# Kernel tuning notes

Hardware: AMD Instinct MI355X
Metric: run time of the kernel (lower is better)

## Reference

```python
import jax, jax.numpy as jnp
import numpy as np

TRAJ_STEPS = 1_000_000


def setup_inputs() -> dict:
    key = jax.random.key(0)
    k1, k2 = jax.random.split(key)
    start_pose = jax.random.normal(k1, (3,), dtype=jnp.float32)
    controls = jax.random.normal(k2, (TRAJ_STEPS, 2), dtype=jnp.float32)
    return {"start_pose": start_pose, "controls": controls}


def reference(start_pose, controls):
    # Unicycle rollout:
    #   traj[0]   = start_pose = (x0, y0, th0)
    #   traj[i+1] = traj[i] + (|u_i0|*cos(th_i), |u_i0|*sin(th_i), 10*u_i1)
    # theta evolves independently of x,y -> closed-form via cumsum.
    th0 = start_pose[2]
    dth = 10.0 * controls[:, 1]                      # (T,)
    th = th0 + jnp.cumsum(dth)                       # theta at steps 1..T
    th_prev = jnp.concatenate([th0[None], th[:-1]])  # theta at steps 0..T-1

    speed = jnp.abs(controls[:, 0])                  # (T,)
    dx = speed * jnp.cos(th_prev)
    dy = speed * jnp.sin(th_prev)
    x = start_pose[0] + jnp.cumsum(dx)               # x at steps 1..T
    y = start_pose[1] + jnp.cumsum(dy)

    traj_tail = jnp.stack([x, y, th], axis=1)        # (T, 3)
    traj = jnp.concatenate([start_pose[None, :], traj_tail], axis=0)  # (T+1, 3)
    return controls, traj
```

## Files before the change

kernel.cpp:

```cpp
#include <hip/hip_runtime.h>
#include <math.h>

#define T_STEPS 1000000
#define BLOCK 256
#define ITEMS 8
#define CHUNK (BLOCK * ITEMS)
#define NB ((T_STEPS + CHUNK - 1) / CHUNK)
#define NF4 (T_STEPS / 2)
#define PER 2


__device__ __forceinline__ double waveScanIncl(double v) {
#pragma unroll
    for (int off = 1; off < 64; off <<= 1) {
        double x = __shfl_up(v, off, 64);
        if ((threadIdx.x & 63) >= off) v += x;
    }
    return v;
}

__device__ __forceinline__ double blockScanEx(double v, double* sw, double* tot) {
    const int lane = threadIdx.x & 63, w = threadIdx.x >> 6;
    double inc = waveScanIncl(v);
    if (lane == 63) sw[w] = inc;
    __syncthreads();
    double w0 = sw[0], w1 = sw[1], w2 = sw[2], w3 = sw[3];
    __syncthreads();
    *tot = w0 + w1 + w2 + w3;
    double woff = (w > 0 ? w0 : 0.0) + (w > 1 ? w1 : 0.0) + (w > 2 ? w2 : 0.0);
    return woff + inc - v;
}

__device__ __forceinline__ double blockSum(double v, double* sw) {
#pragma unroll
    for (int off = 32; off > 0; off >>= 1) v += __shfl_xor(v, off, 64);
    const int lane = threadIdx.x & 63, w = threadIdx.x >> 6;
    if (lane == 0) sw[w] = v;
    __syncthreads();
    double r = sw[0] + sw[1] + sw[2] + sw[3];
    __syncthreads();
    return r;
}

__device__ __forceinline__ void ftrig(double th, double& cs, double& sn) {
    const double INV2PI = 0.15915494309189535;
    double rev = th * INV2PI;
    double fr = rev - rint(rev);
    float x = (float)fr * 6.283185307179586f;
    sn = (double)__sinf(x);
    cs = (double)__cosf(x);
}


__global__ void __launch_bounds__(BLOCK) k_agg(
    const float4* __restrict__ ctrl4, float4* __restrict__ out4,
    double* __restrict__ aggTh, double* __restrict__ aggA,
    double* __restrict__ aggB) {
    __shared__ double sw[4];
    const int b = blockIdx.x, t = threadIdx.x;
    const int f0 = b * (CHUNK / 2) + t * (ITEMS / 2);

    float4 c4[ITEMS / 2];
#pragma unroll
    for (int j = 0; j < ITEMS / 2; ++j) {
        int f = f0 + j;
        c4[j] = (f < NF4) ? ctrl4[f] : make_float4(0.f, 0.f, 0.f, 0.f);
    }
#pragma unroll
    for (int j = 0; j < ITEMS / 2; ++j) {
        int f = f0 + j;
        if (f < NF4) out4[f] = c4[j];
    }

    double dth[ITEMS];
    double lth = 0.0;
#pragma unroll
    for (int j = 0; j < ITEMS / 2; ++j) {
        dth[2 * j]     = 10.0 * (double)c4[j].y;
        dth[2 * j + 1] = 10.0 * (double)c4[j].w;
        lth += dth[2 * j] + dth[2 * j + 1];
    }
    double thTot;
    double thb = blockScanEx(lth, sw, &thTot);

    double la = 0.0, lb = 0.0;
    {
        double run = thb;
#pragma unroll
        for (int j = 0; j < ITEMS / 2; ++j) {
            double s0 = fabs((double)c4[j].x);
            double s1 = fabs((double)c4[j].z);
            double cs, sn;
            ftrig(run, cs, sn);
            la += s0 * cs; lb += s0 * sn;
            run += dth[2 * j];
            ftrig(run, cs, sn);
            la += s1 * cs; lb += s1 * sn;
            run += dth[2 * j + 1];
        }
    }
    double A = blockSum(la, sw);
    double B = blockSum(lb, sw);
    if (t == 0) {
        aggTh[b] = thTot;
        aggA[b]  = A;
        aggB[b]  = B;
    }
}


__global__ void __launch_bounds__(BLOCK) k_out(
    const float4* __restrict__ ctrl4, const float* __restrict__ sp,
    const double* __restrict__ aggTh, const double* __restrict__ aggA,
    const double* __restrict__ aggB, float* __restrict__ traj) {
    __shared__ double sw[4];
    const int b = blockIdx.x, t = threadIdx.x;

    const double x0 = (double)sp[0], y0 = (double)sp[1], th0 = (double)sp[2];

    double pTh[PER], pA[PER], pB[PER];
    double lsum = 0.0;
#pragma unroll
    for (int k = 0; k < PER; ++k) {
        int p = t * PER + k;
        if (p < NB) {
            pTh[k] = aggTh[p];
            pA[k]  = aggA[p];
            pB[k]  = aggB[p];
        } else {
            pTh[k] = pA[k] = pB[k] = 0.0;
        }
        lsum += pTh[k];
    }
    double dummyTot;
    double excl = blockScanEx(lsum, sw, &dummyTot);

    double cx = 0.0, cy = 0.0, mth = 0.0;
    {
        double run = th0 + excl;
#pragma unroll
        for (int k = 0; k < PER; ++k) {
            int p = t * PER + k;
            if (p < b) {
                double cs, sn;
                ftrig(run, cs, sn);
                cx += cs * pA[k] - sn * pB[k];
                cy += sn * pA[k] + cs * pB[k];
                mth += pTh[k];
            }
            run += pTh[k];
        }
    }
    const double psi = th0 + blockSum(mth, sw);
    const double Xin = x0 + blockSum(cx, sw);
    const double Yin = y0 + blockSum(cy, sw);
    double cps, sps;
    ftrig(psi, cps, sps);

    const int f0 = b * (CHUNK / 2) + t * (ITEMS / 2);
    float4 c4[ITEMS / 2];
#pragma unroll
    for (int j = 0; j < ITEMS / 2; ++j) {
        int f = f0 + j;
        c4[j] = (f < NF4) ? ctrl4[f] : make_float4(0.f, 0.f, 0.f, 0.f);
    }
    double dth[ITEMS];
    double lth = 0.0;
#pragma unroll
    for (int j = 0; j < ITEMS / 2; ++j) {
        dth[2 * j]     = 10.0 * (double)c4[j].y;
        dth[2 * j + 1] = 10.0 * (double)c4[j].w;
        lth += dth[2 * j] + dth[2 * j + 1];
    }
    double thTot;
    double thb = blockScanEx(lth, sw, &thTot);

    double av[ITEMS], bv[ITEMS];
    double la = 0.0, lb = 0.0;
    {
        double run = thb;
#pragma unroll
        for (int j = 0; j < ITEMS / 2; ++j) {
            double s0 = fabs((double)c4[j].x);
            double s1 = fabs((double)c4[j].z);
            double cs, sn;
            ftrig(run, cs, sn);
            av[2 * j] = s0 * cs; bv[2 * j] = s0 * sn;
            run += dth[2 * j];
            ftrig(run, cs, sn);
            av[2 * j + 1] = s1 * cs; bv[2 * j + 1] = s1 * sn;
            run += dth[2 * j + 1];
            la += av[2 * j] + av[2 * j + 1];
            lb += bv[2 * j] + bv[2 * j + 1];
        }
    }
    double aTot, bTot;
    double Ar = blockScanEx(la, sw, &aTot);
    double Br = blockScanEx(lb, sw, &bTot);

    {
        const long e0 = (long)b * CHUNK + (long)t * ITEMS;
        double run = thb;
#pragma unroll
        for (int k = 0; k < ITEMS; ++k) {
            Ar += av[k];
            Br += bv[k];
            run += dth[k];
            long i = e0 + k;
            if (i < T_STEPS) {
                float* row = traj + 3 * (i + 1);
                row[0] = (float)(Xin + cps * Ar - sps * Br);
                row[1] = (float)(Yin + sps * Ar + cps * Br);
                row[2] = (float)(psi + run);
            }
        }
    }
    if (b == 0 && t == 0) {
        traj[0] = sp[0];
        traj[1] = sp[1];
        traj[2] = sp[2];
    }
}


extern "C" void kernel_launch(void* const* d_in, const int* in_sizes, int n_in,
                              void* d_out, int out_size, void* d_ws, size_t ws_size,
                              hipStream_t stream) {
    const float*  start_pose = (const float*)d_in[0];
    const float4* ctrl4      = (const float4*)d_in[1];

    float*  out  = (float*)d_out;
    float4* out4 = (float4*)out;
    float*  traj = out + 2 * (long)T_STEPS;

    double* bsum  = (double*)d_ws;
    double* aggTh = bsum;
    double* aggA  = aggTh + NB;
    double* aggB  = aggA + NB;

    hipLaunchKernelGGL(k_agg, dim3(NB), dim3(BLOCK), 0, stream,
                       ctrl4, out4, aggTh, aggA, aggB);
    hipLaunchKernelGGL(k_out, dim3(NB), dim3(BLOCK), 0, stream,
                       ctrl4, start_pose, aggTh, aggA, aggB, traj);
}
```

Measured before the change: 23.46 us.

## Fuse aggregate and output kernels into one cooperative kernel with grid sync

Merges the two-pass scan (per-block aggregate kernel, then output kernel) into a single cooperative launch separated by a grid-wide sync. Each block keeps its controls, theta scan and per-element cos/sin products in registers across the sync, so the second pass no longer reloads controls or recomputes trig. This drops one kernel launch and the duplicated work. In exchange it relies on all 489 blocks being co-resident (launch_bounds with 2 blocks per CU) and pays the cost of a grid barrier.

```diff
diff --git a/kernel.cpp b/kernel.cpp
--- a/kernel.cpp
+++ b/kernel.cpp
@@ -1,5 +1,8 @@
 #include <hip/hip_runtime.h>
+#include <hip/hip_cooperative_groups.h>
 #include <math.h>
+
+namespace cg = cooperative_groups;
 
 #define T_STEPS 1000000
 #define BLOCK 256
@@ -52,8 +55,9 @@
 }
 
 
-__global__ void __launch_bounds__(BLOCK) k_agg(
-    const float4* __restrict__ ctrl4, float4* __restrict__ out4,
+__global__ void __launch_bounds__(BLOCK, 2) k_fused(
+    const float4* __restrict__ ctrl4, const float* __restrict__ sp,
+    float4* __restrict__ out4, float* __restrict__ traj,
     double* __restrict__ aggTh, double* __restrict__ aggA,
     double* __restrict__ aggB) {
     __shared__ double sw[4];
@@ -72,98 +76,6 @@
         if (f < NF4) out4[f] = c4[j];
     }
 
-    double dth[ITEMS];
-    double lth = 0.0;
-#pragma unroll
-    for (int j = 0; j < ITEMS / 2; ++j) {
-        dth[2 * j]     = 10.0 * (double)c4[j].y;
-        dth[2 * j + 1] = 10.0 * (double)c4[j].w;
-        lth += dth[2 * j] + dth[2 * j + 1];
-    }
-    double thTot;
-    double thb = blockScanEx(lth, sw, &thTot);
-
-    double la = 0.0, lb = 0.0;
-    {
-        double run = thb;
-#pragma unroll
-        for (int j = 0; j < ITEMS / 2; ++j) {
-            double s0 = fabs((double)c4[j].x);
-            double s1 = fabs((double)c4[j].z);
-            double cs, sn;
-            ftrig(run, cs, sn);
-            la += s0 * cs; lb += s0 * sn;
-            run += dth[2 * j];
-            ftrig(run, cs, sn);
-            la += s1 * cs; lb += s1 * sn;
-            run += dth[2 * j + 1];
-        }
-    }
-    double A = blockSum(la, sw);
-    double B = blockSum(lb, sw);
-    if (t == 0) {
-        aggTh[b] = thTot;
-        aggA[b]  = A;
-        aggB[b]  = B;
-    }
-}
-
-
-__global__ void __launch_bounds__(BLOCK) k_out(
-    const float4* __restrict__ ctrl4, const float* __restrict__ sp,
-    const double* __restrict__ aggTh, const double* __restrict__ aggA,
-    const double* __restrict__ aggB, float* __restrict__ traj) {
-    __shared__ double sw[4];
-    const int b = blockIdx.x, t = threadIdx.x;
-
-    const double x0 = (double)sp[0], y0 = (double)sp[1], th0 = (double)sp[2];
-
-    double pTh[PER], pA[PER], pB[PER];
-    double lsum = 0.0;
-#pragma unroll
-    for (int k = 0; k < PER; ++k) {
-        int p = t * PER + k;
-        if (p < NB) {
-            pTh[k] = aggTh[p];
-            pA[k]  = aggA[p];
-            pB[k]  = aggB[p];
-        } else {
-            pTh[k] = pA[k] = pB[k] = 0.0;
-        }
-        lsum += pTh[k];
-    }
-    double dummyTot;
-    double excl = blockScanEx(lsum, sw, &dummyTot);
-
-    double cx = 0.0, cy = 0.0, mth = 0.0;
-    {
-        double run = th0 + excl;
-#pragma unroll
-        for (int k = 0; k < PER; ++k) {
-            int p = t * PER + k;
-            if (p < b) {
-                double cs, sn;
-                ftrig(run, cs, sn);
-                cx += cs * pA[k] - sn * pB[k];
-                cy += sn * pA[k] + cs * pB[k];
-                mth += pTh[k];
-            }
-            run += pTh[k];
-        }
-    }
-    const double psi = th0 + blockSum(mth, sw);
-    const double Xin = x0 + blockSum(cx, sw);
-    const double Yin = y0 + blockSum(cy, sw);
-    double cps, sps;
-    ftrig(psi, cps, sps);
-
-    const int f0 = b * (CHUNK / 2) + t * (ITEMS / 2);
-    float4 c4[ITEMS / 2];
-#pragma unroll
-    for (int j = 0; j < ITEMS / 2; ++j) {
-        int f = f0 + j;
-        c4[j] = (f < NF4) ? ctrl4[f] : make_float4(0.f, 0.f, 0.f, 0.f);
-    }
     double dth[ITEMS];
     double lth = 0.0;
 #pragma unroll
@@ -194,6 +106,57 @@
             lb += bv[2 * j] + bv[2 * j + 1];
         }
     }
+    double A = blockSum(la, sw);
+    double B = blockSum(lb, sw);
+    if (t == 0) {
+        aggTh[b] = thTot;
+        aggA[b]  = A;
+        aggB[b]  = B;
+    }
+
+    cg::this_grid().sync();
+
+    const double x0 = (double)sp[0], y0 = (double)sp[1], th0 = (double)sp[2];
+
+    double pTh[PER], pA[PER], pB[PER];
+    double lsum = 0.0;
+#pragma unroll
+    for (int k = 0; k < PER; ++k) {
+        int p = t * PER + k;
+        if (p < NB) {
+            pTh[k] = aggTh[p];
+            pA[k]  = aggA[p];
+            pB[k]  = aggB[p];
+        } else {
+            pTh[k] = pA[k] = pB[k] = 0.0;
+        }
+        lsum += pTh[k];
+    }
+    double dummyTot;
+    double excl = blockScanEx(lsum, sw, &dummyTot);
+
+    double cx = 0.0, cy = 0.0, mth = 0.0;
+    {
+        double run2 = th0 + excl;
+#pragma unroll
+        for (int k = 0; k < PER; ++k) {
+            int p = t * PER + k;
+            if (p < b) {
+                double cs, sn;
+                ftrig(run2, cs, sn);
+                cx += cs * pA[k] - sn * pB[k];
+                cy += sn * pA[k] + cs * pB[k];
+                mth += pTh[k];
+            }
+            run2 += pTh[k];
+        }
+    }
+    const double psi = th0 + blockSum(mth, sw);
+    const double Xin = x0 + blockSum(cx, sw);
+    const double Yin = y0 + blockSum(cy, sw);
+    double cps, sps;
+    ftrig(psi, cps, sps);
+
     double aTot, bTot;
     double Ar = blockScanEx(la, sw, &aTot);
     double Br = blockScanEx(lb, sw, &bTot);
@@ -233,13 +196,14 @@
     float4* out4 = (float4*)out;
     float*  traj = out + 2 * (long)T_STEPS;
 
-    double* bsum  = (double*)d_ws;
-    double* aggTh = bsum;
+    double* aggTh = (double*)d_ws;
     double* aggA  = aggTh + NB;
     double* aggB  = aggA + NB;
 
-    hipLaunchKernelGGL(k_agg, dim3(NB), dim3(BLOCK), 0, stream,
-                       ctrl4, out4, aggTh, aggA, aggB);
-    hipLaunchKernelGGL(k_out, dim3(NB), dim3(BLOCK), 0, stream,
-                       ctrl4, start_pose, aggTh, aggA, aggB, traj);
-}
+    void* kargs[] = {
+        (void*)&ctrl4, (void*)&start_pose, (void*)&out4, (void*)&traj,
+        (void*)&aggTh, (void*)&aggA, (void*)&aggB
+    };
+    hipLaunchCooperativeKernel((const void*)k_fused, dim3(NB), dim3(BLOCK),
+                               kargs, 0, stream);
+}
```

Measured after the change: 64.41 us. 174% more time.
